# Performance work log

Hardware: AMD Instinct MI355X
Metric: run time of the kernel (lower is better)

The kernel has to match this reference:

```python
import jax, jax.numpy as jnp
import numpy as np

N_NODES = 100000
N_EDGES = 1_600_000
D_IN = 128
D_OUT = 128


def setup_inputs() -> dict:
    key = jax.random.key(0)
    k1, k2, k3, k4 = jax.random.split(key, 4)
    x = jax.random.normal(k1, (N_NODES, D_IN), dtype=jnp.float32)
    adj = jax.random.randint(k2, (2, N_EDGES), 0, N_NODES, dtype=jnp.int64)
    # eqx.nn.Linear-style init: U(-1/sqrt(in), 1/sqrt(in))
    lim = 1.0 / np.sqrt(D_IN)
    W = jax.random.uniform(k3, (D_OUT, D_IN), minval=-lim, maxval=lim, dtype=jnp.float32)
    b = jax.random.uniform(k4, (D_OUT,), minval=-lim, maxval=lim, dtype=jnp.float32)
    return {"x": x, "adj": adj, "W": W, "b": b}


def reference(x, adj, W, b):
    n = x.shape[0]
    s, r = adj[0], adj[1]
    ones = jnp.ones(s.shape, dtype=x.dtype)
    sender_degree = jax.ops.segment_sum(ones, s, num_segments=n)    # [n]
    receiver_degree = jax.ops.segment_sum(ones, r, num_segments=n)  # [n]
    # linear (dropout is identity at p=0)
    h = x @ W.T + b                                                 # [n, D_OUT]
    # symmetric degree normalization: rescale senders, scatter-add to receivers, rescale receivers
    h = h * jax.lax.rsqrt(jnp.maximum(sender_degree, 1.0))[:, None]
    h = jax.ops.segment_sum(h[s], r, num_segments=n)                # gather + scatter-add
    h = h * jax.lax.rsqrt(jnp.maximum(receiver_degree, 1.0))[:, None]
    h = jax.nn.silu(h)
    return (h, adj)
```

## Files before the change

kernel.cpp:

```cpp
#include <hip/hip_runtime.h>
#include <hip/hip_bf16.h>
#include <hip/hip_fp16.h>

typedef __attribute__((ext_vector_type(8))) short short8;
typedef __attribute__((ext_vector_type(4))) float floatx4;

#define DFEAT 128
#define BCAP 5120
#define WSTR 136
#define MAXNBK 400

__device__ __forceinline__ int clampi(int v, int lo, int hi) {
    return v < lo ? lo : (v > hi ? hi : v);
}
__device__ __forceinline__ ushort f2bf(float f) {
    unsigned u = __float_as_uint(f);
    unsigned r = (u + 0x7FFFu + ((u >> 16) & 1u)) >> 16;
    return (ushort)r;
}
__device__ __forceinline__ float bf2f(ushort u) {
    return __uint_as_float(((unsigned)u) << 16);
}
__device__ __forceinline__ float h16tof(ushort hb) {
    __half_raw hr; hr.x = hb;
    return __half2float((__half)hr);
}
__device__ __forceinline__ unsigned f2bf8_sw(float f) {
    __half h = __float2half(f);
    __half_raw hr = (__half_raw)h;
    unsigned u = (unsigned)hr.x;
    return (u + 0x7Fu + ((u >> 8) & 1u)) >> 8;
}
__device__ __forceinline__ unsigned packbf8x4(float4 v) {
#if __has_builtin(__builtin_amdgcn_cvt_pk_bf8_f32)
    int lo = __builtin_amdgcn_cvt_pk_bf8_f32(v.x, v.y, 0, false);
    int full = __builtin_amdgcn_cvt_pk_bf8_f32(v.z, v.w, lo, true);
    return (unsigned)full;
#else
    return f2bf8_sw(v.x) | (f2bf8_sw(v.y) << 8) | (f2bf8_sw(v.z) << 16) | (f2bf8_sw(v.w) << 24);
#endif
}
__device__ __forceinline__ float2 bf8x2tof(int w) {
#if __has_builtin(__builtin_amdgcn_cvt_pk_f32_bf8)
    typedef __attribute__((ext_vector_type(2))) float f2v;
    f2v r = __builtin_amdgcn_cvt_pk_f32_bf8(w, false);
    float2 o; o.x = r[0]; o.y = r[1];
    return o;
#else
    float2 o;
    o.x = h16tof((ushort)((w & 0xFF) << 8));
    o.y = h16tof((ushort)(w & 0xFF00));
    return o;
#endif
}

__device__ __forceinline__ int ldS(const int* adj, int f, int E, int e) {
    return f ? adj[2 * (size_t)e] : adj[e];
}
__device__ __forceinline__ int ldR(const int* adj, int f, int E, int e) {
    return f ? adj[2 * ((size_t)E + e)] : adj[(size_t)E + e];
}

__global__ __launch_bounds__(512) void k_front(const float* __restrict__ x,
                                               unsigned* __restrict__ xs, int n32, int staged,
                                               const float* __restrict__ W, unsigned* __restrict__ Wb,
                                               const int* __restrict__ adj, int* __restrict__ flag_g,
                                               int* __restrict__ scur, int* __restrict__ rcur,
                                               unsigned char* __restrict__ sbuf, unsigned* __restrict__ rbuf,
                                               int E, int N, int NBK, int SG) {
    int t = threadIdx.x;
    int b = blockIdx.x;
    if (b < SG) {
        if (b == 0) {
            for (int i = t; i < 8192; i += 512) {
                float2 v = ((const float2*)W)[i];
                Wb[i] = (unsigned)f2bf(v.x) | ((unsigned)f2bf(v.y) << 16);
            }
        }
        if (staged) {
            int stride = SG * 512;
            for (int i = b * 512 + t; i < n32; i += stride)
                xs[i] = packbf8x4(((const float4*)x)[i]);
        }
        return;
    }
    __shared__ int hs[8 * MAXNBK], hr[8 * MAXNBK];
    __shared__ int bs[MAXNBK], br[MAXNBK];
    __shared__ int fsh;
    int pb = b - SG;
    int PB = gridDim.x - SG;
    int wv = t >> 6, ln = t & 63;
    if (t < 64) {
        int nz = 0;
        for (int i = t; i < 256; i += 64) nz |= adj[2 * i + 1];
        #pragma unroll
        for (int off = 32; off > 0; off >>= 1) nz |= __shfl_down(nz, off);
        if (t == 0) { fsh = (nz == 0) ? 1 : 0; if (pb == 0) flag_g[0] = fsh; }
    }
    for (int i = t; i < 8 * MAXNBK; i += 512) { hs[i] = 0; hr[i] = 0; }
    __syncthreads();
    int f = fsh;
    int chunk = (E + PB - 1) / PB;
    int e0 = pb * chunk;
    int e1 = min(E, e0 + chunk);
    int span = e1 - e0;
    int wper = (span + 7) >> 3;
    int a0 = e0 + wv * wper;
    int a1 = min(e1, a0 + wper);
    int* mys = &hs[wv * MAXNBK];
    int* myr = &hr[wv * MAXNBK];
    for (int e = a0 + ln; e < a1; e += 64) {
        int s = clampi(ldS(adj, f, E, e), 0, N - 1);
        int r = clampi(ldR(adj, f, E, e), 0, N - 1);
        atomicAdd(&mys[s >> 8], 1);
        atomicAdd(&myr[r >> 8], 1);
    }
    __syncthreads();
    for (int i = t; i < NBK; i += 512) {
        int aS = 0, aR = 0;
        #pragma unroll
        for (int w = 0; w < 8; ++w) {
            int vS = hs[w * MAXNBK + i]; hs[w * MAXNBK + i] = aS; aS += vS;
            int vR = hr[w * MAXNBK + i]; hr[w * MAXNBK + i] = aR; aR += vR;
        }
        bs[i] = aS ? atomicAdd(&scur[i], aS) : 0;
        br[i] = aR ? atomicAdd(&rcur[i], aR) : 0;
    }
    __syncthreads();
    for (int e = a0 + ln; e < a1; e += 64) {
        int s = clampi(ldS(adj, f, E, e), 0, N - 1);
        int r = clampi(ldR(adj, f, E, e), 0, N - 1);
        int ps = bs[s >> 8] + atomicAdd(&mys[s >> 8], 1);
        if (ps < BCAP) sbuf[(size_t)(s >> 8) * BCAP + ps] = (unsigned char)(s & 255);
        int pr = br[r >> 8] + atomicAdd(&myr[r >> 8], 1);
        if (pr < BCAP) rbuf[(size_t)(r >> 8) * BCAP + pr] = ((unsigned)(r & 255) << 17) | (unsigned)s;
    }
}

__global__ __launch_bounds__(256) void k_invs(const unsigned char* __restrict__ sbuf,
                                              const int* __restrict__ scur,
                                              float* __restrict__ inv_s, int N) {
    __shared__ int h[256];
    int b = blockIdx.x, t = threadIdx.x;
    int sc = min(scur[b], BCAP);
    const unsigned char* sb = sbuf + (size_t)b * BCAP;
    h[t] = 0;
    __syncthreads();
    for (int i = t; i < sc; i += 256) atomicAdd(&h[sb[i]], 1);
    __syncthreads();
    int node = (b << 8) + t;
    if (node < N) inv_s[node] = rsqrtf(fmaxf((float)h[t], 1.0f));
}

__global__ __launch_bounds__(256) void k_sort(unsigned* __restrict__ rbuf,
                                              const int* __restrict__ rcur,
                                              const float* __restrict__ inv_s,
                                              int* __restrict__ deg_r, int* __restrict__ startv,
                                              int N) {
    __shared__ __align__(16) unsigned pk[BCAP];
    __shared__ int h[256], off[256];
    int b = blockIdx.x, t = threadIdx.x;
    int node = (b << 8) + t;
    int cnt = min(rcur[b], BCAP);
    unsigned* rb = rbuf + (size_t)b * BCAP;
    int cnt4 = cnt >> 2;
    const uint4* rb4 = (const uint4*)rb;
    for (int i = t; i < cnt4; i += 256) ((uint4*)pk)[i] = rb4[i];
    for (int i = (cnt4 << 2) + t; i < cnt; i += 256) pk[i] = rb[i];
    h[t] = 0;
    __syncthreads();
    for (int i = t; i < cnt; i += 256) atomicAdd(&h[pk[i] >> 17], 1);
    __syncthreads();
    int hv = h[t];
    off[t] = hv;
    __syncthreads();
    for (int o = 1; o < 256; o <<= 1) {
        int v = (t >= o) ? off[t - o] : 0;
        __syncthreads();
        off[t] += v;
        __syncthreads();
    }
    int excl = off[t] - hv;
    if (node < N) { deg_r[node] = hv; startv[node] = b * BCAP + excl; }
    __syncthreads();
    h[t] = excl;
    __syncthreads();
    for (int i = t; i < cnt; i += 256) {
        unsigned v = pk[i];
        int s = (int)(v & 0x1FFFFu);
        unsigned iv8 = f2bf8_sw(inv_s[clampi(s, 0, N - 1)]);
        int pos = atomicAdd(&h[v >> 17], 1);
        if (pos >= 0 && pos < cnt) rb[pos] = (v & 0x1FFFFu) | (iv8 << 24);
    }
}

__global__ __launch_bounds__(512) void k_back(const ushort* __restrict__ xs,
                                              const float* __restrict__ bias,
                                              const unsigned* __restrict__ Wb,
                                              const int* __restrict__ startv,
                                              const int* __restrict__ deg_r,
                                              const unsigned* __restrict__ esrc,
                                              float* __restrict__ out0, int N, int RB, int ntiles,
                                              const int* __restrict__ adj, const int* __restrict__ flag,
                                              float* __restrict__ out1, int n1) {
    __shared__ ushort Wt[128 * WSTR];
    __shared__ ushort At[32 * WSTR];
    __shared__ float csrow[32], invrow[32];
    int tid = threadIdx.x;

    if ((int)blockIdx.x >= ntiles) {
        int f = flag[0];
        int nb = gridDim.x - ntiles;
        for (int i = ((int)blockIdx.x - ntiles) * 512 + tid; i < n1; i += nb * 512) {
            int v = f ? adj[2 * (size_t)i] : adj[i];
            out1[i] = bf2f(f2bf((float)v));
        }
        return;
    }

    int m0 = blockIdx.x * 32;
    for (int i = tid; i < 8192; i += 512) {
        unsigned v = Wb[i];
        int row = i >> 6, col = (2 * i) & 127;
        *(unsigned*)(&Wt[row * WSTR + col]) = v;
    }

    int w = tid >> 6, d = tid & 63;
    #pragma unroll 1
    for (int k = 0; k < 4; ++k) {
        int nl = w * 4 + k;
        int node = m0 + nl;
        int cnt = 0, base = 0;
        if (node < N) {
            cnt = clampi(deg_r[node], 0, BCAP);
            base = clampi(startv[node], 0, RB - cnt);
        }
        cnt = __builtin_amdgcn_readfirstlane(cnt);
        base = __builtin_amdgcn_readfirstlane(base);
        const unsigned* ep = esrc + base;
        float a0 = 0.f, a1 = 0.f, cs = 0.f;
        int j = 0;
        for (; j + 7 < cnt; j += 8) {
            unsigned q0 = ep[j],     q1 = ep[j + 1], q2 = ep[j + 2], q3 = ep[j + 3];
            unsigned q4 = ep[j + 4], q5 = ep[j + 5], q6 = ep[j + 6], q7 = ep[j + 7];
            int r0 = (int)xs[((q0 & 0x1FFFFu) << 6) + d];
            int r1 = (int)xs[((q1 & 0x1FFFFu) << 6) + d];
            int r2 = (int)xs[((q2 & 0x1FFFFu) << 6) + d];
            int r3 = (int)xs[((q3 & 0x1FFFFu) << 6) + d];
            int r4 = (int)xs[((q4 & 0x1FFFFu) << 6) + d];
            int r5 = (int)xs[((q5 & 0x1FFFFu) << 6) + d];
            int r6 = (int)xs[((q6 & 0x1FFFFu) << 6) + d];
            int r7 = (int)xs[((q7 & 0x1FFFFu) << 6) + d];
            float v0 = h16tof((ushort)((q0 >> 16) & 0xFF00u));
            float v1 = h16tof((ushort)((q1 >> 16) & 0xFF00u));
            float v2 = h16tof((ushort)((q2 >> 16) & 0xFF00u));
            float v3 = h16tof((ushort)((q3 >> 16) & 0xFF00u));
            float v4 = h16tof((ushort)((q4 >> 16) & 0xFF00u));
            float v5 = h16tof((ushort)((q5 >> 16) & 0xFF00u));
            float v6 = h16tof((ushort)((q6 >> 16) & 0xFF00u));
            float v7 = h16tof((ushort)((q7 >> 16) & 0xFF00u));
            float2 f0 = bf8x2tof(r0), f1 = bf8x2tof(r1), f2 = bf8x2tof(r2), f3 = bf8x2tof(r3);
            float2 f4 = bf8x2tof(r4), f5 = bf8x2tof(r5), f6 = bf8x2tof(r6), f7 = bf8x2tof(r7);
            a0 += v0 * f0.x; a1 += v0 * f0.y;
            a0 += v1 * f1.x; a1 += v1 * f1.y;
            a0 += v2 * f2.x; a1 += v2 * f2.y;
            a0 += v3 * f3.x; a1 += v3 * f3.y;
            a0 += v4 * f4.x; a1 += v4 * f4.y;
            a0 += v5 * f5.x; a1 += v5 * f5.y;
            a0 += v6 * f6.x; a1 += v6 * f6.y;
            a0 += v7 * f7.x; a1 += v7 * f7.y;
            cs += ((v0 + v1) + (v2 + v3)) + ((v4 + v5) + (v6 + v7));
        }
        for (; j < cnt; ++j) {
            unsigned q0 = ep[j];
            float v0 = h16tof((ushort)((q0 >> 16) & 0xFF00u));
            float2 f0 = bf8x2tof((int)xs[((q0 & 0x1FFFFu) << 6) + d]);
            a0 += v0 * f0.x; a1 += v0 * f0.y;
            cs += v0;
        }
        ushort2 p; p.x = f2bf(a0); p.y = f2bf(a1);
        *(ushort2*)(&At[nl * WSTR + 2 * d]) = p;
        if (d == 0) {
            csrow[nl] = cs;
            invrow[nl] = rsqrtf(fmaxf((float)cnt, 1.0f));
        }
    }
    __syncthreads();

    int quad = d >> 4, r16 = d & 15;
    int rt = w & 1;
    short8 a[4];
    #pragma unroll
    for (int g = 0; g < 4; ++g)
        a[g] = *(const short8*)(&At[(rt * 16 + r16) * WSTR + g * 32 + quad * 8]);

    #pragma unroll
    for (int half = 0; half < 2; ++half) {
        int ct = (w >> 1) + half * 4;
        floatx4 acc = {0.f, 0.f, 0.f, 0.f};
        #pragma unroll
        for (int g = 0; g < 4; ++g) {
            short8 bb = *(const short8*)(&Wt[(ct * 16 + r16) * WSTR + g * 32 + quad * 8]);
            acc = __builtin_amdgcn_mfma_f32_16x16x32_bf16(a[g], bb, acc, 0, 0, 0);
        }
        int dcol = ct * 16 + r16;
        float bc = bias[dcol];
        #pragma unroll
        for (int g = 0; g < 4; ++g) {
            int ml = rt * 16 + quad * 4 + g;
            int grow = m0 + ml;
            if (grow < N) {
                float v = (acc[g] + csrow[ml] * bc) * invrow[ml];
                float z = v / (1.0f + __expf(-v));
                if (!(z > -50.0f && z < 50.0f)) z = 0.0f;
                out0[(size_t)grow * DFEAT + dcol] = z;
            }
        }
    }
}

__global__ __launch_bounds__(256) void k_aggregate_fb(const float* __restrict__ x,
                                                      const int* __restrict__ startv,
                                                      const int* __restrict__ deg_r,
                                                      const unsigned* __restrict__ esrc,
                                                      float* __restrict__ xa,
                                                      float* __restrict__ cvec, int N, int RB) {
    int node = blockIdx.x * 4 + (threadIdx.x >> 6);
    int d = threadIdx.x & 63;
    if (node >= N) return;
    int cnt = clampi(deg_r[node], 0, BCAP);
    int base = clampi(startv[node], 0, RB - cnt);
    cnt = __builtin_amdgcn_readfirstlane(cnt);
    base = __builtin_amdgcn_readfirstlane(base);
    const unsigned* ep = esrc + base;
    float a0 = 0.f, a1 = 0.f, cs = 0.f;
    for (int j = 0; j < cnt; ++j) {
        unsigned w0 = ep[j];
        int s0 = (int)(w0 & 0x1FFFFu);
        float v0 = h16tof((ushort)((w0 >> 16) & 0xFF00u));
        float2 f0 = ((const float2*)x)[(size_t)s0 * 64 + d];
        a0 += v0 * f0.x; a1 += v0 * f0.y;
        cs += v0;
    }
    float2 o; o.x = a0; o.y = a1;
    ((float2*)xa)[(size_t)node * 64 + d] = o;
    if (d == 0) cvec[node] = cs;
}

__global__ __launch_bounds__(256) void k_matmul_fb(float* __restrict__ xa,
                                                   const unsigned* __restrict__ Wb,
                                                   const float* __restrict__ bias,
                                                   const float* __restrict__ c,
                                                   const int* __restrict__ deg_r, int M) {
    __shared__ ushort Wt[128 * WSTR];
    __shared__ ushort At[64 * WSTR];
    int tid = threadIdx.x;
    int m0 = blockIdx.x * 64;
    for (int i = tid; i < 8192; i += 256) {
        unsigned v = Wb[i];
        int row = i >> 6, col = (2 * i) & 127;
        *(unsigned*)(&Wt[row * WSTR + col]) = v;
    }
    for (int i = tid; i < 4096; i += 256) {
        int row = i >> 6, col = (2 * i) & 127;
        int grow = m0 + row;
        float2 v;
        if (grow < M) v = ((const float2*)xa)[(size_t)grow * 64 + (col >> 1)];
        else { v.x = 0.f; v.y = 0.f; }
        ushort2 p; p.x = f2bf(v.x); p.y = f2bf(v.y);
        *(ushort2*)(&At[row * WSTR + col]) = p;
    }
    __syncthreads();
    int wid = tid >> 6, lane = tid & 63;
    int quad = lane >> 4, r16 = lane & 15;
    short8 a[4];
    #pragma unroll
    for (int g = 0; g < 4; ++g)
        a[g] = *(const short8*)(&At[(wid * 16 + r16) * WSTR + g * 32 + quad * 8]);
    int rbl = wid * 16 + quad * 4;
    float cg[4], invr[4];
    #pragma unroll
    for (int g = 0; g < 4; ++g) {
        int row = min(m0 + rbl + g, M - 1);
        cg[g] = c[row];
        invr[g] = rsqrtf(fmaxf((float)deg_r[row], 1.0f));
    }
    #pragma unroll
    for (int nt = 0; nt < 8; ++nt) {
        floatx4 acc = {0.f, 0.f, 0.f, 0.f};
        #pragma unroll
        for (int g = 0; g < 4; ++g) {
            short8 bb = *(const short8*)(&Wt[(nt * 16 + r16) * WSTR + g * 32 + quad * 8]);
            acc = __builtin_amdgcn_mfma_f32_16x16x32_bf16(a[g], bb, acc, 0, 0, 0);
        }
        int dcol = nt * 16 + r16;
        float bc = bias[dcol];
        #pragma unroll
        for (int g = 0; g < 4; ++g) {
            int grow = m0 + rbl + g;
            if (grow < M) {
                float v = (acc[g] + cg[g] * bc) * invr[g];
                float z = v / (1.0f + __expf(-v));
                if (!(z > -50.0f && z < 50.0f)) z = 0.0f;
                xa[(size_t)grow * DFEAT + dcol] = z;
            }
        }
    }
}

__global__ void k_adjcopy(const int* __restrict__ adj, const int* __restrict__ flag,
                          float* __restrict__ out, int n) {
    int i = blockIdx.x * 256 + threadIdx.x;
    if (i >= n) return;
    int f = flag[0];
    int v = f ? adj[2 * (size_t)i] : adj[i];
    out[i] = bf2f(f2bf((float)v));
}

extern "C" void kernel_launch(void* const* d_in, const int* in_sizes, int n_in,
                              void* d_out, int out_size, void* d_ws, size_t ws_size,
                              hipStream_t stream) {
    const float* x    = (const float*)d_in[0];
    const int*   adj  = (const int*)d_in[1];
    const float* W    = (const float*)d_in[2];
    const float* bias = (const float*)d_in[3];

    const int N = in_sizes[0] / DFEAT;
    const int E = (out_size - N * DFEAT) / 2;
    const int NBK = (N + 255) >> 8;
    const int N4 = ((N + 255) / 256) * 256;
    const int RB = NBK * BCAP;

    float* out  = (float*)d_out;
    float* out0 = out;
    float* out1 = out + (size_t)N * DFEAT;

    size_t xsB  = (size_t)N * DFEAT;
    size_t sbB  = ((size_t)NBK * BCAP + 255) & ~(size_t)255;
    size_t rbB  = (size_t)RB * 4;
    size_t metaB = (size_t)N4 * 16 + 8192;
    size_t need = xsB + sbB + rbB + metaB + 32768;
    int staged = (ws_size >= need) ? 1 : 0;

    unsigned char* sbuf;
    unsigned* rbuf;
    char* csr;
    ushort* xs = (ushort*)d_ws;
    if (staged) {
        sbuf = (unsigned char*)d_ws + xsB;
        rbuf = (unsigned*)((char*)d_ws + xsB + sbB);
        csr  = (char*)d_ws + xsB + sbB + rbB;
    } else {
        sbuf = (unsigned char*)d_out;
        rbuf = (unsigned*)out1;
        csr  = (char*)out1 + rbB;
    }
    float* inv_s  = (float*)csr;
    int*   deg_r  = (int*)(csr + (size_t)N4 * 4);
    int*   startv = (int*)(csr + (size_t)N4 * 8);
    float* cvec   = (float*)(csr + (size_t)N4 * 12);
    int*   bkt    = (int*)(csr + (size_t)N4 * 16);
    unsigned* Wb  = (unsigned*)(csr + metaB);
    int *scur = bkt, *rcur = bkt + 512, *flag = bkt + 1024;

    hipMemsetAsync(bkt, 0, 1028 * 4, stream);

    int SG = staged ? 512 : 1;
    int PB = 256;
    k_front<<<SG + PB, 512, 0, stream>>>(x, (unsigned*)xs, N * 32, staged, W, Wb, adj, flag,
                                         scur, rcur, sbuf, rbuf, E, N, NBK, SG);
    k_invs<<<NBK, 256, 0, stream>>>(sbuf, scur, inv_s, N);
    k_sort<<<NBK, 256, 0, stream>>>(rbuf, rcur, inv_s, deg_r, startv, N);

    if (staged) {
        int ntiles = (N + 31) / 32;
        k_back<<<ntiles + 256, 512, 0, stream>>>(xs, bias, Wb, startv, deg_r, rbuf,
                                                 out0, N, RB, ntiles, adj, flag, out1, 2 * E);
    } else {
        k_aggregate_fb<<<(N + 3) / 4, 256, 0, stream>>>(x, startv, deg_r, rbuf, out0, cvec, N, RB);
        k_matmul_fb<<<(N + 63) / 64, 256, 0, stream>>>(out0, Wb, bias, cvec, deg_r, N);
        k_adjcopy<<<(2 * E + 255) / 256, 256, 0, stream>>>(adj, flag, out1, 2 * E);
    }
}
```

Before: 236.1 us.

## Build receiver CSR via global degree histogram, scan, and atomic scatter

```diff
diff --git a/kernel.cpp b/kernel.cpp
--- a/kernel.cpp
+++ b/kernel.cpp
@@ -61,13 +61,13 @@
     return f ? adj[2 * ((size_t)E + e)] : adj[(size_t)E + e];
 }
 
-__global__ __launch_bounds__(512) void k_front(const float* __restrict__ x,
-                                               unsigned* __restrict__ xs, int n32, int staged,
-                                               const float* __restrict__ W, unsigned* __restrict__ Wb,
-                                               const int* __restrict__ adj, int* __restrict__ flag_g,
-                                               int* __restrict__ scur, int* __restrict__ rcur,
-                                               unsigned char* __restrict__ sbuf, unsigned* __restrict__ rbuf,
-                                               int E, int N, int NBK, int SG) {
+
+__global__ __launch_bounds__(512) void k_hist(const float* __restrict__ x,
+                                              unsigned* __restrict__ xs, int n32,
+                                              const float* __restrict__ W, unsigned* __restrict__ Wb,
+                                              const int* __restrict__ adj, int* __restrict__ flag_g,
+                                              int* __restrict__ deg_s, int* __restrict__ deg_r,
+                                              int E, int N, int SG) {
     int t = threadIdx.x;
     int b = blockIdx.x;
     if (b < SG) {
@@ -77,19 +77,14 @@
                 Wb[i] = (unsigned)f2bf(v.x) | ((unsigned)f2bf(v.y) << 16);
             }
         }
-        if (staged) {
-            int stride = SG * 512;
-            for (int i = b * 512 + t; i < n32; i += stride)
-                xs[i] = packbf8x4(((const float4*)x)[i]);
-        }
+        int stride = SG * 512;
+        for (int i = b * 512 + t; i < n32; i += stride)
+            xs[i] = packbf8x4(((const float4*)x)[i]);
         return;
     }
-    __shared__ int hs[8 * MAXNBK], hr[8 * MAXNBK];
-    __shared__ int bs[MAXNBK], br[MAXNBK];
     __shared__ int fsh;
     int pb = b - SG;
     int PB = gridDim.x - SG;
-    int wv = t >> 6, ln = t & 63;
     if (t < 64) {
         int nz = 0;
         for (int i = t; i < 256; i += 64) nz |= adj[2 * i + 1];
@@ -97,112 +92,93 @@
         for (int off = 32; off > 0; off >>= 1) nz |= __shfl_down(nz, off);
         if (t == 0) { fsh = (nz == 0) ? 1 : 0; if (pb == 0) flag_g[0] = fsh; }
     }
-    for (int i = t; i < 8 * MAXNBK; i += 512) { hs[i] = 0; hr[i] = 0; }
     __syncthreads();
     int f = fsh;
     int chunk = (E + PB - 1) / PB;
     int e0 = pb * chunk;
     int e1 = min(E, e0 + chunk);
-    int span = e1 - e0;
-    int wper = (span + 7) >> 3;
-    int a0 = e0 + wv * wper;
-    int a1 = min(e1, a0 + wper);
-    int* mys = &hs[wv * MAXNBK];
-    int* myr = &hr[wv * MAXNBK];
-    for (int e = a0 + ln; e < a1; e += 64) {
+    for (int e = e0 + t; e < e1; e += 512) {
         int s = clampi(ldS(adj, f, E, e), 0, N - 1);
         int r = clampi(ldR(adj, f, E, e), 0, N - 1);
-        atomicAdd(&mys[s >> 8], 1);
-        atomicAdd(&myr[r >> 8], 1);
-    }
-    __syncthreads();
-    for (int i = t; i < NBK; i += 512) {
-        int aS = 0, aR = 0;
-        #pragma unroll
-        for (int w = 0; w < 8; ++w) {
-            int vS = hs[w * MAXNBK + i]; hs[w * MAXNBK + i] = aS; aS += vS;
-            int vR = hr[w * MAXNBK + i]; hr[w * MAXNBK + i] = aR; aR += vR;
-        }
-        bs[i] = aS ? atomicAdd(&scur[i], aS) : 0;
-        br[i] = aR ? atomicAdd(&rcur[i], aR) : 0;
-    }
-    __syncthreads();
-    for (int e = a0 + ln; e < a1; e += 64) {
+        atomicAdd(&deg_s[s], 1);
+        atomicAdd(&deg_r[r], 1);
+    }
+}
+
+__global__ __launch_bounds__(256) void k_scan1(const int* __restrict__ deg_r,
+                                               const int* __restrict__ deg_s,
+                                               int* __restrict__ svl, int* __restrict__ cur,
+                                               float* __restrict__ inv_s,
+                                               int* __restrict__ psum, int N) {
+    __shared__ int sh[256];
+    int b = blockIdx.x, t = threadIdx.x;
+    int node = (b << 8) + t;
+    int v = (node < N) ? deg_r[node] : 0;
+    sh[t] = v;
+    __syncthreads();
+    for (int o = 1; o < 256; o <<= 1) {
+        int u = (t >= o) ? sh[t - o] : 0;
+        __syncthreads();
+        sh[t] += u;
+        __syncthreads();
+    }
+    int excl = sh[t] - v;
+    if (node < N) {
+        svl[node] = excl;
+        cur[node] = 0;
+        inv_s[node] = rsqrtf(fmaxf((float)deg_s[node], 1.0f));
+    }
+    if (t == 255) psum[b] = sh[255];
+}
+
+__global__ __launch_bounds__(512) void k_scan2(int* __restrict__ psum, int NB) {
+    __shared__ int sh[512];
+    int t = threadIdx.x;
+    int v = (t < NB) ? psum[t] : 0;
+    sh[t] = v;
+    __syncthreads();
+    for (int o = 1; o < 512; o <<= 1) {
+        int u = (t >= o) ? sh[t - o] : 0;
+        __syncthreads();
+        sh[t] += u;
+        __syncthreads();
+    }
+    if (t < NB) psum[t] = sh[t] - v;
+}
+
+__global__ __launch_bounds__(512) void k_scatter(const int* __restrict__ adj,
+                                                 const int* __restrict__ flag,
+                                                 const float* __restrict__ inv_s,
+                                                 const int* __restrict__ psum,
+                                                 const int* __restrict__ svl,
+                                                 int* __restrict__ cur,
+                                                 unsigned* __restrict__ rbuf, int E, int N) {
+    int t = threadIdx.x;
+    int pb = blockIdx.x;
+    int PB = gridDim.x;
+    int f = flag[0];
+    int chunk = (E + PB - 1) / PB;
+    int e0 = pb * chunk;
+    int e1 = min(E, e0 + chunk);
+    for (int e = e0 + t; e < e1; e += 512) {
         int s = clampi(ldS(adj, f, E, e), 0, N - 1);
         int r = clampi(ldR(adj, f, E, e), 0, N - 1);
-        int ps = bs[s >> 8] + atomicAdd(&mys[s >> 8], 1);
-        if (ps < BCAP) sbuf[(size_t)(s >> 8) * BCAP + ps] = (unsigned char)(s & 255);
-        int pr = br[r >> 8] + atomicAdd(&myr[r >> 8], 1);
-        if (pr < BCAP) rbuf[(size_t)(r >> 8) * BCAP + pr] = ((unsigned)(r & 255) << 17) | (unsigned)s;
-    }
-}
-
-__global__ __launch_bounds__(256) void k_invs(const unsigned char* __restrict__ sbuf,
-                                              const int* __restrict__ scur,
-                                              float* __restrict__ inv_s, int N) {
-    __shared__ int h[256];
-    int b = blockIdx.x, t = threadIdx.x;
-    int sc = min(scur[b], BCAP);
-    const unsigned char* sb = sbuf + (size_t)b * BCAP;
-    h[t] = 0;
-    __syncthreads();
-    for (int i = t; i < sc; i += 256) atomicAdd(&h[sb[i]], 1);
-    __syncthreads();
-    int node = (b << 8) + t;
-    if (node < N) inv_s[node] = rsqrtf(fmaxf((float)h[t], 1.0f));
-}
-
-__global__ __launch_bounds__(256) void k_sort(unsigned* __restrict__ rbuf,
-                                              const int* __restrict__ rcur,
-                                              const float* __restrict__ inv_s,
-                                              int* __restrict__ deg_r, int* __restrict__ startv,
-                                              int N) {
-    __shared__ __align__(16) unsigned pk[BCAP];
-    __shared__ int h[256], off[256];
-    int b = blockIdx.x, t = threadIdx.x;
-    int node = (b << 8) + t;
-    int cnt = min(rcur[b], BCAP);
-    unsigned* rb = rbuf + (size_t)b * BCAP;
-    int cnt4 = cnt >> 2;
-    const uint4* rb4 = (const uint4*)rb;
-    for (int i = t; i < cnt4; i += 256) ((uint4*)pk)[i] = rb4[i];
-    for (int i = (cnt4 << 2) + t; i < cnt; i += 256) pk[i] = rb[i];
-    h[t] = 0;
-    __syncthreads();
-    for (int i = t; i < cnt; i += 256) atomicAdd(&h[pk[i] >> 17], 1);
-    __syncthreads();
-    int hv = h[t];
-    off[t] = hv;
-    __syncthreads();
-    for (int o = 1; o < 256; o <<= 1) {
-        int v = (t >= o) ? off[t - o] : 0;
-        __syncthreads();
-        off[t] += v;
-        __syncthreads();
-    }
-    int excl = off[t] - hv;
-    if (node < N) { deg_r[node] = hv; startv[node] = b * BCAP + excl; }
-    __syncthreads();
-    h[t] = excl;
-    __syncthreads();
-    for (int i = t; i < cnt; i += 256) {
-        unsigned v = pk[i];
-        int s = (int)(v & 0x1FFFFu);
-        unsigned iv8 = f2bf8_sw(inv_s[clampi(s, 0, N - 1)]);
-        int pos = atomicAdd(&h[v >> 17], 1);
-        if (pos >= 0 && pos < cnt) rb[pos] = (v & 0x1FFFFu) | (iv8 << 24);
-    }
-}
-
-__global__ __launch_bounds__(512) void k_back(const ushort* __restrict__ xs,
-                                              const float* __restrict__ bias,
-                                              const unsigned* __restrict__ Wb,
-                                              const int* __restrict__ startv,
-                                              const int* __restrict__ deg_r,
-                                              const unsigned* __restrict__ esrc,
-                                              float* __restrict__ out0, int N, int RB, int ntiles,
-                                              const int* __restrict__ adj, const int* __restrict__ flag,
-                                              float* __restrict__ out1, int n1) {
+        unsigned iv8 = f2bf8_sw(inv_s[s]);
+        int pos = psum[r >> 8] + svl[r] + atomicAdd(&cur[r], 1);
+        if (pos >= 0 && pos < E) rbuf[pos] = (unsigned)s | (iv8 << 24);
+    }
+}
+
+__global__ __launch_bounds__(512) void k_back_g(const ushort* __restrict__ xs,
+                                                const float* __restrict__ bias,
+                                                const unsigned* __restrict__ Wb,
+                                                const int* __restrict__ svl,
+                                                const int* __restrict__ psum,
+                                                const int* __restrict__ deg_r,
+                                                const unsigned* __restrict__ esrc,
+                                                float* __restrict__ out0, int N, int RB, int ntiles,
+                                                const int* __restrict__ adj, const int* __restrict__ flag,
+                                                float* __restrict__ out1, int n1) {
     __shared__ ushort Wt[128 * WSTR];
     __shared__ ushort At[32 * WSTR];
     __shared__ float csrow[32], invrow[32];
@@ -233,7 +209,7 @@
         int cnt = 0, base = 0;
         if (node < N) {
             cnt = clampi(deg_r[node], 0, BCAP);
-            base = clampi(startv[node], 0, RB - cnt);
+            base = clampi(svl[node] + psum[node >> 8], 0, RB - cnt);
         }
         cnt = __builtin_amdgcn_readfirstlane(cnt);
         base = __builtin_amdgcn_readfirstlane(base);
@@ -319,6 +295,139 @@
     }
 }
 
+__global__ __launch_bounds__(512) void k_front(const float* __restrict__ x,
+                                               unsigned* __restrict__ xs, int n32, int staged,
+                                               const float* __restrict__ W, unsigned* __restrict__ Wb,
+                                               const int* __restrict__ adj, int* __restrict__ flag_g,
+                                               int* __restrict__ scur, int* __restrict__ rcur,
+                                               unsigned char* __restrict__ sbuf, unsigned* __restrict__ rbuf,
+                                               int E, int N, int NBK, int SG) {
+    int t = threadIdx.x;
+    int b = blockIdx.x;
+    if (b < SG) {
+        if (b == 0) {
+            for (int i = t; i < 8192; i += 512) {
+                float2 v = ((const float2*)W)[i];
+                Wb[i] = (unsigned)f2bf(v.x) | ((unsigned)f2bf(v.y) << 16);
+            }
+        }
+        if (staged) {
+            int stride = SG * 512;
+            for (int i = b * 512 + t; i < n32; i += stride)
+                xs[i] = packbf8x4(((const float4*)x)[i]);
+        }
+        return;
+    }
+    __shared__ int hs[8 * MAXNBK], hr[8 * MAXNBK];
+    __shared__ int bs[MAXNBK], br[MAXNBK];
+    __shared__ int fsh;
+    int pb = b - SG;
+    int PB = gridDim.x - SG;
+    int wv = t >> 6, ln = t & 63;
+    if (t < 64) {
+        int nz = 0;
+        for (int i = t; i < 256; i += 64) nz |= adj[2 * i + 1];
+        #pragma unroll
+        for (int off = 32; off > 0; off >>= 1) nz |= __shfl_down(nz, off);
+        if (t == 0) { fsh = (nz == 0) ? 1 : 0; if (pb == 0) flag_g[0] = fsh; }
+    }
+    for (int i = t; i < 8 * MAXNBK; i += 512) { hs[i] = 0; hr[i] = 0; }
+    __syncthreads();
+    int f = fsh;
+    int chunk = (E + PB - 1) / PB;
+    int e0 = pb * chunk;
+    int e1 = min(E, e0 + chunk);
+    int span = e1 - e0;
+    int wper = (span + 7) >> 3;
+    int a0 = e0 + wv * wper;
+    int a1 = min(e1, a0 + wper);
+    int* mys = &hs[wv * MAXNBK];
+    int* myr = &hr[wv * MAXNBK];
+    for (int e = a0 + ln; e < a1; e += 64) {
+        int s = clampi(ldS(adj, f, E, e), 0, N - 1);
+        int r = clampi(ldR(adj, f, E, e), 0, N - 1);
+        atomicAdd(&mys[s >> 8], 1);
+        atomicAdd(&myr[r >> 8], 1);
+    }
+    __syncthreads();
+    for (int i = t; i < NBK; i += 512) {
+        int aS = 0, aR = 0;
+        #pragma unroll
+        for (int w = 0; w < 8; ++w) {
+            int vS = hs[w * MAXNBK + i]; hs[w * MAXNBK + i] = aS; aS += vS;
+            int vR = hr[w * MAXNBK + i]; hr[w * MAXNBK + i] = aR; aR += vR;
+        }
+        bs[i] = aS ? atomicAdd(&scur[i], aS) : 0;
+        br[i] = aR ? atomicAdd(&rcur[i], aR) : 0;
+    }
+    __syncthreads();
+    for (int e = a0 + ln; e < a1; e += 64) {
+        int s = clampi(ldS(adj, f, E, e), 0, N - 1);
+        int r = clampi(ldR(adj, f, E, e), 0, N - 1);
+        int ps = bs[s >> 8] + atomicAdd(&mys[s >> 8], 1);
+        if (ps < BCAP) sbuf[(size_t)(s >> 8) * BCAP + ps] = (unsigned char)(s & 255);
+        int pr = br[r >> 8] + atomicAdd(&myr[r >> 8], 1);
+        if (pr < BCAP) rbuf[(size_t)(r >> 8) * BCAP + pr] = ((unsigned)(r & 255) << 17) | (unsigned)s;
+    }
+}
+
+__global__ __launch_bounds__(256) void k_invs(const unsigned char* __restrict__ sbuf,
+                                              const int* __restrict__ scur,
+                                              float* __restrict__ inv_s, int N) {
+    __shared__ int h[256];
+    int b = blockIdx.x, t = threadIdx.x;
+    int sc = min(scur[b], BCAP);
+    const unsigned char* sb = sbuf + (size_t)b * BCAP;
+    h[t] = 0;
+    __syncthreads();
+    for (int i = t; i < sc; i += 256) atomicAdd(&h[sb[i]], 1);
+    __syncthreads();
+    int node = (b << 8) + t;
+    if (node < N) inv_s[node] = rsqrtf(fmaxf((float)h[t], 1.0f));
+}
+
+__global__ __launch_bounds__(256) void k_sort(unsigned* __restrict__ rbuf,
+                                              const int* __restrict__ rcur,
+                                              const float* __restrict__ inv_s,
+                                              int* __restrict__ deg_r, int* __restrict__ startv,
+                                              int N) {
+    __shared__ __align__(16) unsigned pk[BCAP];
+    __shared__ int h[256], off[256];
+    int b = blockIdx.x, t = threadIdx.x;
+    int node = (b << 8) + t;
+    int cnt = min(rcur[b], BCAP);
+    unsigned* rb = rbuf + (size_t)b * BCAP;
+    int cnt4 = cnt >> 2;
+    const uint4* rb4 = (const uint4*)rb;
+    for (int i = t; i < cnt4; i += 256) ((uint4*)pk)[i] = rb4[i];
+    for (int i = (cnt4 << 2) + t; i < cnt; i += 256) pk[i] = rb[i];
+    h[t] = 0;
+    __syncthreads();
+    for (int i = t; i < cnt; i += 256) atomicAdd(&h[pk[i] >> 17], 1);
+    __syncthreads();
+    int hv = h[t];
+    off[t] = hv;
+    __syncthreads();
+    for (int o = 1; o < 256; o <<= 1) {
+        int v = (t >= o) ? off[t - o] : 0;
+        __syncthreads();
+        off[t] += v;
+        __syncthreads();
+    }
+    int excl = off[t] - hv;
+    if (node < N) { deg_r[node] = hv; startv[node] = b * BCAP + excl; }
+    __syncthreads();
+    h[t] = excl;
+    __syncthreads();
+    for (int i = t; i < cnt; i += 256) {
+        unsigned v = pk[i];
+        int s = (int)(v & 0x1FFFFu);
+        unsigned iv8 = f2bf8_sw(inv_s[clampi(s, 0, N - 1)]);
+        int pos = atomicAdd(&h[v >> 17], 1);
+        if (pos >= 0 && pos < cnt) rb[pos] = (v & 0x1FFFFu) | (iv8 << 24);
+    }
+}
+
 __global__ __launch_bounds__(256) void k_aggregate_fb(const float* __restrict__ x,
                                                       const int* __restrict__ startv,
                                                       const int* __restrict__ deg_r,
@@ -429,56 +538,68 @@
     const int E = (out_size - N * DFEAT) / 2;
     const int NBK = (N + 255) >> 8;
     const int N4 = ((N + 255) / 256) * 256;
-    const int RB = NBK * BCAP;
 
     float* out  = (float*)d_out;
     float* out0 = out;
     float* out1 = out + (size_t)N * DFEAT;
 
-    size_t xsB  = (size_t)N * DFEAT;
-    size_t sbB  = ((size_t)NBK * BCAP + 255) & ~(size_t)255;
-    size_t rbB  = (size_t)RB * 4;
-    size_t metaB = (size_t)N4 * 16 + 8192;
-    size_t need = xsB + sbB + rbB + metaB + 32768;
+    size_t xsB   = (size_t)N * DFEAT;
+    size_t rbB   = (size_t)E * 4;
+    size_t metaB = (size_t)N4 * 20 + 8192 + 32768;
+    size_t need  = xsB + rbB + metaB + 4096;
     int staged = (ws_size >= need) ? 1 : 0;
 
-    unsigned char* sbuf;
-    unsigned* rbuf;
-    char* csr;
-    ushort* xs = (ushort*)d_ws;
     if (staged) {
-        sbuf = (unsigned char*)d_ws + xsB;
-        rbuf = (unsigned*)((char*)d_ws + xsB + sbB);
-        csr  = (char*)d_ws + xsB + sbB + rbB;
-    } else {
-        sbuf = (unsigned char*)d_out;
-        rbuf = (unsigned*)out1;
-        csr  = (char*)out1 + rbB;
-    }
+        ushort* xs = (ushort*)d_ws;
+        unsigned* rbuf = (unsigned*)((char*)d_ws + xsB);
+        char* csr = (char*)d_ws + xsB + rbB;
+        int*   deg_s = (int*)csr;
+        int*   deg_r = deg_s + N4;
+        int*   svl   = deg_r + N4;
+        int*   cur   = svl + N4;
+        float* inv_s = (float*)(cur + N4);
+        int*   psum  = (int*)(inv_s + N4);
+        int*   flag  = psum + 512;
+        unsigned* Wb = (unsigned*)(flag + 512);
+
+        hipMemsetAsync(deg_s, 0, (size_t)N4 * 8, stream);
+
+        int SG = 512, PB = 256;
+        k_hist<<<SG + PB, 512, 0, stream>>>(x, (unsigned*)xs, N * 32, W, Wb, adj, flag,
+                                            deg_s, deg_r, E, N, SG);
+        k_scan1<<<NBK, 256, 0, stream>>>(deg_r, deg_s, svl, cur, inv_s, psum, N);
+        k_scan2<<<1, 512, 0, stream>>>(psum, NBK);
+        k_scatter<<<256, 512, 0, stream>>>(adj, flag, inv_s, psum, svl, cur, rbuf, E, N);
+        int ntiles = (N + 31) / 32;
+        k_back_g<<<ntiles + 256, 512, 0, stream>>>(xs, bias, Wb, svl, psum, deg_r, rbuf,
+                                                   out0, N, E, ntiles, adj, flag, out1, 2 * E);
+        return;
+    }
+
+    const int RB = NBK * BCAP;
+    size_t sbB = ((size_t)NBK * BCAP + 255) & ~(size_t)255;
+    size_t rbBf = (size_t)RB * 4;
+    size_t metaBf = (size_t)N4 * 16 + 8192;
+    unsigned char* sbuf = (unsigned char*)d_out;
+    unsigned* rbuf = (unsigned*)out1;
+    char* csr = (char*)out1 + rbBf;
+    (void)sbB; (void)metaBf;
     float* inv_s  = (float*)csr;
     int*   deg_r  = (int*)(csr + (size_t)N4 * 4);
     int*   startv = (int*)(csr + (size_t)N4 * 8);
     float* cvec   = (float*)(csr + (size_t)N4 * 12);
     int*   bkt    = (int*)(csr + (size_t)N4 * 16);
-    unsigned* Wb  = (unsigned*)(csr + metaB);
+    unsigned* Wb  = (unsigned*)(csr + (size_t)N4 * 16 + 8192);
     int *scur = bkt, *rcur = bkt + 512, *flag = bkt + 1024;
 
     hipMemsetAsync(bkt, 0, 1028 * 4, stream);
 
-    int SG = staged ? 512 : 1;
-    int PB = 256;
-    k_front<<<SG + PB, 512, 0, stream>>>(x, (unsigned*)xs, N * 32, staged, W, Wb, adj, flag,
+    int SG = 1, PB = 256;
+    k_front<<<SG + PB, 512, 0, stream>>>(x, (unsigned*)d_ws, N * 32, 0, W, Wb, adj, flag,
                                          scur, rcur, sbuf, rbuf, E, N, NBK, SG);
     k_invs<<<NBK, 256, 0, stream>>>(sbuf, scur, inv_s, N);
     k_sort<<<NBK, 256, 0, stream>>>(rbuf, rcur, inv_s, deg_r, startv, N);
-
-    if (staged) {
-        int ntiles = (N + 31) / 32;
-        k_back<<<ntiles + 256, 512, 0, stream>>>(xs, bias, Wb, startv, deg_r, rbuf,
-                                                 out0, N, RB, ntiles, adj, flag, out1, 2 * E);
-    } else {
-        k_aggregate_fb<<<(N + 3) / 4, 256, 0, stream>>>(x, startv, deg_r, rbuf, out0, cvec, N, RB);
-        k_matmul_fb<<<(N + 63) / 64, 256, 0, stream>>>(out0, Wb, bias, cvec, deg_r, N);
-        k_adjcopy<<<(2 * E + 255) / 256, 256, 0, stream>>>(adj, flag, out1, 2 * E);
-    }
-}
+    k_aggregate_fb<<<(N + 3) / 4, 256, 0, stream>>>(x, startv, deg_r, rbuf, out0, cvec, N, RB);
+    k_matmul_fb<<<(N + 63) / 64, 256, 0, stream>>>(out0, Wb, bias, cvec, deg_r, N);
+    k_adjcopy<<<(2 * E + 255) / 256, 256, 0, stream>>>(adj, flag, out1, 2 * E);
+}
```

New measurement: 382.9 us. 1.62x slower.

## Interleave gathers for four nodes per wave and use nontemporal output stores

Applied to the files above, without the earlier changes.

```diff
diff --git a/kernel.cpp b/kernel.cpp
--- a/kernel.cpp
+++ b/kernel.cpp
@@ -213,7 +213,7 @@
         int nb = gridDim.x - ntiles;
         for (int i = ((int)blockIdx.x - ntiles) * 512 + tid; i < n1; i += nb * 512) {
             int v = f ? adj[2 * (size_t)i] : adj[i];
-            out1[i] = bf2f(f2bf((float)v));
+            __builtin_nontemporal_store(bf2f(f2bf((float)v)), &out1[i]);
         }
         return;
     }
@@ -226,63 +226,64 @@
     }
 
     int w = tid >> 6, d = tid & 63;
-    #pragma unroll 1
+    int cntk[4], basek[4];
+    #pragma unroll
+    for (int k = 0; k < 4; ++k) {
+        int node = m0 + w * 4 + k;
+        int c = 0, bse = 0;
+        if (node < N) {
+            c = clampi(deg_r[node], 0, BCAP);
+            bse = clampi(startv[node], 0, RB - (c > 0 ? c : 1));
+        }
+        cntk[k] = __builtin_amdgcn_readfirstlane(c);
+        basek[k] = __builtin_amdgcn_readfirstlane(bse);
+    }
+    int cmax = max(max(cntk[0], cntk[1]), max(cntk[2], cntk[3]));
+    float A0[4] = {0.f, 0.f, 0.f, 0.f};
+    float A1[4] = {0.f, 0.f, 0.f, 0.f};
+    float CS[4] = {0.f, 0.f, 0.f, 0.f};
+
+    for (int j = 0; j < cmax; j += 4) {
+        unsigned qv[4][4];
+        #pragma unroll
+        for (int k = 0; k < 4; ++k) {
+            #pragma unroll
+            for (int t2 = 0; t2 < 4; ++t2) {
+                int idx = j + t2;
+                int lim = cntk[k] - 1;
+                if (lim < 0) lim = 0;
+                if (idx > lim) idx = lim;
+                qv[k][t2] = esrc[basek[k] + idx];
+            }
+        }
+        int rv[4][4];
+        #pragma unroll
+        for (int k = 0; k < 4; ++k) {
+            #pragma unroll
+            for (int t2 = 0; t2 < 4; ++t2)
+                rv[k][t2] = (int)xs[((qv[k][t2] & 0x1FFFFu) << 6) + d];
+        }
+        #pragma unroll
+        for (int k = 0; k < 4; ++k) {
+            #pragma unroll
+            for (int t2 = 0; t2 < 4; ++t2) {
+                float v = ((j + t2) < cntk[k]) ? h16tof((ushort)((qv[k][t2] >> 16) & 0xFF00u)) : 0.f;
+                float2 f2v_ = bf8x2tof(rv[k][t2]);
+                A0[k] += v * f2v_.x;
+                A1[k] += v * f2v_.y;
+                CS[k] += v;
+            }
+        }
+    }
+
+    #pragma unroll
     for (int k = 0; k < 4; ++k) {
         int nl = w * 4 + k;
-        int node = m0 + nl;
-        int cnt = 0, base = 0;
-        if (node < N) {
-            cnt = clampi(deg_r[node], 0, BCAP);
-            base = clampi(startv[node], 0, RB - cnt);
-        }
-        cnt = __builtin_amdgcn_readfirstlane(cnt);
-        base = __builtin_amdgcn_readfirstlane(base);
-        const unsigned* ep = esrc + base;
-        float a0 = 0.f, a1 = 0.f, cs = 0.f;
-        int j = 0;
-        for (; j + 7 < cnt; j += 8) {
-            unsigned q0 = ep[j],     q1 = ep[j + 1], q2 = ep[j + 2], q3 = ep[j + 3];
-            unsigned q4 = ep[j + 4], q5 = ep[j + 5], q6 = ep[j + 6], q7 = ep[j + 7];
-            int r0 = (int)xs[((q0 & 0x1FFFFu) << 6) + d];
-            int r1 = (int)xs[((q1 & 0x1FFFFu) << 6) + d];
-            int r2 = (int)xs[((q2 & 0x1FFFFu) << 6) + d];
-            int r3 = (int)xs[((q3 & 0x1FFFFu) << 6) + d];
-            int r4 = (int)xs[((q4 & 0x1FFFFu) << 6) + d];
-            int r5 = (int)xs[((q5 & 0x1FFFFu) << 6) + d];
-            int r6 = (int)xs[((q6 & 0x1FFFFu) << 6) + d];
-            int r7 = (int)xs[((q7 & 0x1FFFFu) << 6) + d];
-            float v0 = h16tof((ushort)((q0 >> 16) & 0xFF00u));
-            float v1 = h16tof((ushort)((q1 >> 16) & 0xFF00u));
-            float v2 = h16tof((ushort)((q2 >> 16) & 0xFF00u));
-            float v3 = h16tof((ushort)((q3 >> 16) & 0xFF00u));
-            float v4 = h16tof((ushort)((q4 >> 16) & 0xFF00u));
-            float v5 = h16tof((ushort)((q5 >> 16) & 0xFF00u));
-            float v6 = h16tof((ushort)((q6 >> 16) & 0xFF00u));
-            float v7 = h16tof((ushort)((q7 >> 16) & 0xFF00u));
-            float2 f0 = bf8x2tof(r0), f1 = bf8x2tof(r1), f2 = bf8x2tof(r2), f3 = bf8x2tof(r3);
-            float2 f4 = bf8x2tof(r4), f5 = bf8x2tof(r5), f6 = bf8x2tof(r6), f7 = bf8x2tof(r7);
-            a0 += v0 * f0.x; a1 += v0 * f0.y;
-            a0 += v1 * f1.x; a1 += v1 * f1.y;
-            a0 += v2 * f2.x; a1 += v2 * f2.y;
-            a0 += v3 * f3.x; a1 += v3 * f3.y;
-            a0 += v4 * f4.x; a1 += v4 * f4.y;
-            a0 += v5 * f5.x; a1 += v5 * f5.y;
-            a0 += v6 * f6.x; a1 += v6 * f6.y;
-            a0 += v7 * f7.x; a1 += v7 * f7.y;
-            cs += ((v0 + v1) + (v2 + v3)) + ((v4 + v5) + (v6 + v7));
-        }
-        for (; j < cnt; ++j) {
-            unsigned q0 = ep[j];
-            float v0 = h16tof((ushort)((q0 >> 16) & 0xFF00u));
-            float2 f0 = bf8x2tof((int)xs[((q0 & 0x1FFFFu) << 6) + d]);
-            a0 += v0 * f0.x; a1 += v0 * f0.y;
-            cs += v0;
-        }
-        ushort2 p; p.x = f2bf(a0); p.y = f2bf(a1);
+        ushort2 p; p.x = f2bf(A0[k]); p.y = f2bf(A1[k]);
         *(ushort2*)(&At[nl * WSTR + 2 * d]) = p;
         if (d == 0) {
-            csrow[nl] = cs;
-            invrow[nl] = rsqrtf(fmaxf((float)cnt, 1.0f));
+            csrow[nl] = CS[k];
+            invrow[nl] = rsqrtf(fmaxf((float)cntk[k], 1.0f));
         }
     }
     __syncthreads();
@@ -313,7 +314,7 @@
                 float v = (acc[g] + csrow[ml] * bc) * invrow[ml];
                 float z = v / (1.0f + __expf(-v));
                 if (!(z > -50.0f && z < 50.0f)) z = 0.0f;
-                out0[(size_t)grow * DFEAT + dcol] = z;
+                __builtin_nontemporal_store(z, &out0[(size_t)grow * DFEAT + dcol]);
             }
         }
     }
```

After: 231.0 us. 2.2% less time.
